# Kernel tuning notes

Measured on AMD Instinct MI355X. Metric: run time of the kernel, lower is better.

## Reference

```python
import jax, jax.numpy as jnp
import numpy as np

FORGET_BIAS = 1.0

def _lstm_step(c, h, x, W, b):
    # TF BasicLSTMCell: concat([x, h]) @ W + b -> split into i, j, f, o
    gates = jnp.concatenate([x, h], axis=-1) @ W + b
    i, j, f, o = jnp.split(gates, 4, axis=-1)
    new_c = c * jax.nn.sigmoid(f + FORGET_BIAS) + jax.nn.sigmoid(i) * jnp.tanh(j)
    new_h = jnp.tanh(new_c) * jax.nn.sigmoid(o)
    return new_c, new_h

def setup_inputs() -> dict:
    key = jax.random.key(0)
    ks = jax.random.split(key, 8)
    B, T, D, H, C = 64, 128, 2048, 512, 101
    s1 = 1.0 / np.sqrt(D + H)
    s2 = 1.0 / np.sqrt(2 * H)
    so = 1.0 / np.sqrt(H)
    return {
        "inputs": jax.random.normal(ks[0], (B, T, D), dtype=jnp.float32),
        "labels": jax.random.randint(ks[1], (B, T), 0, C, dtype=jnp.int64),
        "W1": jax.random.normal(ks[2], (D + H, 4 * H), dtype=jnp.float32) * s1,
        "b1": jnp.zeros((4 * H,), dtype=jnp.float32),
        "W2": jax.random.normal(ks[3], (2 * H, 4 * H), dtype=jnp.float32) * s2,
        "b2": jnp.zeros((4 * H,), dtype=jnp.float32),
        "Wout": jax.random.normal(ks[4], (H, C), dtype=jnp.float32) * so,
        "bout": jnp.zeros((C,), dtype=jnp.float32),
    }

def reference(inputs, labels, W1, b1, W2, b2, Wout, bout):
    B, T, D = inputs.shape
    H = Wout.shape[0]

    def step(carry, x_t):
        (c1, h1), (c2, h2) = carry
        c1, h1 = _lstm_step(c1, h1, x_t, W1, b1)
        c2, h2 = _lstm_step(c2, h2, h1, W2, b2)
        return ((c1, h1), (c2, h2)), h2

    zeros = jnp.zeros((B, H), dtype=inputs.dtype)
    init = ((zeros, zeros), (zeros, zeros))
    xs = jnp.swapaxes(inputs, 0, 1)  # [T, B, D]
    _, hs = jax.lax.scan(step, init, xs)  # hs: [T, B, H]
    outputs = jnp.swapaxes(hs, 0, 1)  # [B, T, H]

    logits = outputs @ Wout + bout  # [B, T, C]
    preds = jax.nn.softmax(logits, axis=-1)
    log_probs = jax.nn.log_softmax(logits, axis=-1)
    ce = -jnp.take_along_axis(log_probs, labels[..., None], axis=-1)[..., 0]  # [B, T]
    cost = jnp.mean(jnp.sum(ce, axis=1))
    return preds, cost
```

## Files before the change

### kernel.cpp

```cpp
#include <hip/hip_runtime.h>
#include <cmath>

#define Bb   64
#define Tt   128
#define Dd   2048
#define Hh   512
#define Gg   2048
#define Cc   101
#define PC   112
#define ROWS 8192

typedef unsigned short u16;
typedef __attribute__((ext_vector_type(8))) short bf16x8;
typedef __attribute__((ext_vector_type(4))) float f32x4;

__device__ __forceinline__ u16 bf16rne(float x) {
  unsigned u = __float_as_uint(x);
  unsigned r = (u + 0x7fffu + ((u >> 16) & 1u)) >> 16;
  return (u16)r;
}
__device__ __forceinline__ void split_bf16(float x, u16& h, u16& l) {
  h = bf16rne(x);
  l = bf16rne(x - __uint_as_float(((unsigned)h) << 16));
}
__device__ __forceinline__ float sigm(float x) { return 1.f / (1.f + expf(-x)); }

__global__ __launch_bounds__(256)
void convert_hilo(const float* __restrict__ src, u16* __restrict__ hi,
                  u16* __restrict__ lo, int n4) {
  for (int i = blockIdx.x * 256 + threadIdx.x; i < n4; i += gridDim.x * 256) {
    const float4 v = ((const float4*)src)[i];
    ushort4 h, l;
    split_bf16(v.x, h.x, l.x);
    split_bf16(v.y, h.y, l.y);
    split_bf16(v.z, h.z, l.z);
    split_bf16(v.w, h.w, l.w);
    ((ushort4*)hi)[i] = h;
    ((ushort4*)lo)[i] = l;
  }
}

__global__ __launch_bounds__(256)
void convertT_w1(const float* __restrict__ W1, u16* __restrict__ Th,
                 u16* __restrict__ Tl) {
  __shared__ float tl[32][33];
  const int tx = threadIdx.x, ty = threadIdx.y;
  const int k0 = blockIdx.x * 32, c0 = blockIdx.y * 32;
#pragma unroll
  for (int j = 0; j < 4; ++j)
    tl[ty + j * 8][tx] = W1[(size_t)(k0 + ty + j * 8) * Gg + (c0 + tx)];
  __syncthreads();
#pragma unroll
  for (int j = 0; j < 4; ++j) {
    const float v = tl[tx][ty + j * 8];
    u16 h, l;
    split_bf16(v, h, l);
    const size_t o = (size_t)(c0 + ty + j * 8) * Dd + (k0 + tx);
    Th[o] = h;
    Tl[o] = l;
  }
}

__global__ __launch_bounds__(256)
void convert_woutT(const float* __restrict__ Wout, u16* __restrict__ Th,
                   u16* __restrict__ Tl) {
  const int c = blockIdx.x;
  for (int k = threadIdx.x; k < Hh; k += 256) {
    const float v = (c < Cc) ? Wout[k * Cc + c] : 0.f;
    u16 h, l;
    split_bf16(v, h, l);
    Th[c * Hh + k] = h;
    Tl[c * Hh + k] = l;
  }
}

__global__ __launch_bounds__(256)
void permuteW(const float* __restrict__ src, u16* __restrict__ dh,
              u16* __restrict__ dl, int K) {
  __shared__ float tl[32][33];
  const int tx = threadIdx.x, ty = threadIdx.y;
  const int k0 = blockIdx.x * 32, c0 = blockIdx.y * 32;
#pragma unroll
  for (int j = 0; j < 4; ++j)
    tl[ty + j * 8][tx] = src[(size_t)(k0 + ty + j * 8) * Gg + (c0 + tx)];
  __syncthreads();
#pragma unroll
  for (int j = 0; j < 4; ++j) {
    const int col = c0 + ty + j * 8;
    const int g = col >> 9, mg = col & 511;
    const int cg = mg >> 2, m = mg & 3;
    const float v = tl[tx][ty + j * 8];
    u16 h, l;
    split_bf16(v, h, l);
    const size_t o = (size_t)(cg * 16 + g * 4 + m) * K + k0 + tx;
    dh[o] = h;
    dl[o] = l;
  }
}

__global__ __launch_bounds__(256)
void gemm1_mfma(const u16* __restrict__ Ah, const u16* __restrict__ Al,
                const u16* __restrict__ Bh, const u16* __restrict__ Bl,
                const float* __restrict__ bias, float* __restrict__ C) {
  __shared__ u16 Ash[128][40];
  __shared__ u16 Asl[128][40];
  __shared__ u16 Bsh[128][40];
  __shared__ u16 Bsl[128][40];
  const int tid  = threadIdx.x;
  const int lane = tid & 63, wave = tid >> 6;
  const int wm = wave >> 1, wn = wave & 1;
  const int l15 = lane & 15, k8 = (lane >> 4) * 8, r4 = (lane >> 4) * 4;
  const int row0 = blockIdx.y * 128, col0 = blockIdx.x * 128;
  const int srow = tid >> 1, sk = (tid & 1) * 16;

  const u16* pAh = Ah + (size_t)(row0 + srow) * Dd + sk;
  const u16* pAl = Al + (size_t)(row0 + srow) * Dd + sk;
  const u16* pBh = Bh + (size_t)(col0 + srow) * Dd + sk;
  const u16* pBl = Bl + (size_t)(col0 + srow) * Dd + sk;

  f32x4 acc[4][4];
#pragma unroll
  for (int i = 0; i < 4; ++i)
#pragma unroll
    for (int j = 0; j < 4; ++j) acc[i][j] = (f32x4){0.f, 0.f, 0.f, 0.f};

  for (int k0 = 0; k0 < Dd; k0 += 32) {
    *(bf16x8*)(&Ash[srow][sk])     = *(const bf16x8*)(pAh + k0);
    *(bf16x8*)(&Ash[srow][sk + 8]) = *(const bf16x8*)(pAh + k0 + 8);
    *(bf16x8*)(&Asl[srow][sk])     = *(const bf16x8*)(pAl + k0);
    *(bf16x8*)(&Asl[srow][sk + 8]) = *(const bf16x8*)(pAl + k0 + 8);
    *(bf16x8*)(&Bsh[srow][sk])     = *(const bf16x8*)(pBh + k0);
    *(bf16x8*)(&Bsh[srow][sk + 8]) = *(const bf16x8*)(pBh + k0 + 8);
    *(bf16x8*)(&Bsl[srow][sk])     = *(const bf16x8*)(pBl + k0);
    *(bf16x8*)(&Bsl[srow][sk + 8]) = *(const bf16x8*)(pBl + k0 + 8);
    __syncthreads();

    bf16x8 afh[4], afl[4], bfh[4], bfl[4];
#pragma unroll
    for (int mt = 0; mt < 4; ++mt) {
      afh[mt] = *(const bf16x8*)(&Ash[wm * 64 + mt * 16 + l15][k8]);
      afl[mt] = *(const bf16x8*)(&Asl[wm * 64 + mt * 16 + l15][k8]);
    }
#pragma unroll
    for (int nt = 0; nt < 4; ++nt) {
      bfh[nt] = *(const bf16x8*)(&Bsh[wn * 64 + nt * 16 + l15][k8]);
      bfl[nt] = *(const bf16x8*)(&Bsl[wn * 64 + nt * 16 + l15][k8]);
    }
#pragma unroll
    for (int mt = 0; mt < 4; ++mt)
#pragma unroll
      for (int nt = 0; nt < 4; ++nt) {
        acc[mt][nt] = __builtin_amdgcn_mfma_f32_16x16x32_bf16(
            afh[mt], bfh[nt], acc[mt][nt], 0, 0, 0);
        acc[mt][nt] = __builtin_amdgcn_mfma_f32_16x16x32_bf16(
            afh[mt], bfl[nt], acc[mt][nt], 0, 0, 0);
        acc[mt][nt] = __builtin_amdgcn_mfma_f32_16x16x32_bf16(
            afl[mt], bfh[nt], acc[mt][nt], 0, 0, 0);
      }
    __syncthreads();
  }

#pragma unroll
  for (int nt = 0; nt < 4; ++nt) {
    const int col = col0 + wn * 64 + nt * 16 + l15;
    const float bj = bias[col];
#pragma unroll
    for (int mt = 0; mt < 4; ++mt) {
      float* Cp = C + (size_t)(row0 + wm * 64 + mt * 16 + r4) * Gg + col;
#pragma unroll
      for (int r = 0; r < 4; ++r)
        Cp[(size_t)r * Gg] = acc[mt][nt][r] + bj;
    }
  }
}

__global__ __launch_bounds__(256)
void gemm_proj(const u16* __restrict__ Ah, const u16* __restrict__ Al,
               const u16* __restrict__ Bh, const u16* __restrict__ Bl,
               const float* __restrict__ bout, float* __restrict__ logits) {
  __shared__ u16 Ash[128][40];
  __shared__ u16 Asl[128][40];
  __shared__ u16 Bsh[PC][40];
  __shared__ u16 Bsl[PC][40];
  const int tid  = threadIdx.x;
  const int lane = tid & 63, wave = tid >> 6;
  const int l15 = lane & 15, k8 = (lane >> 4) * 8, r4 = (lane >> 4) * 4;
  const int row0 = blockIdx.x * 128;
  const int srow = tid >> 1, sk = (tid & 1) * 16;

  const u16* pAh = Ah + (size_t)(row0 + srow) * Hh + sk;
  const u16* pAl = Al + (size_t)(row0 + srow) * Hh + sk;
  const u16* pBh = Bh + (size_t)srow * Hh + sk;
  const u16* pBl = Bl + (size_t)srow * Hh + sk;

  f32x4 acc[2][7];
#pragma unroll
  for (int i = 0; i < 2; ++i)
#pragma unroll
    for (int j = 0; j < 7; ++j) acc[i][j] = (f32x4){0.f, 0.f, 0.f, 0.f};

  for (int k0 = 0; k0 < Hh; k0 += 32) {
    *(bf16x8*)(&Ash[srow][sk])     = *(const bf16x8*)(pAh + k0);
    *(bf16x8*)(&Ash[srow][sk + 8]) = *(const bf16x8*)(pAh + k0 + 8);
    *(bf16x8*)(&Asl[srow][sk])     = *(const bf16x8*)(pAl + k0);
    *(bf16x8*)(&Asl[srow][sk + 8]) = *(const bf16x8*)(pAl + k0 + 8);
    if (srow < PC) {
      *(bf16x8*)(&Bsh[srow][sk])     = *(const bf16x8*)(pBh + k0);
      *(bf16x8*)(&Bsh[srow][sk + 8]) = *(const bf16x8*)(pBh + k0 + 8);
      *(bf16x8*)(&Bsl[srow][sk])     = *(const bf16x8*)(pBl + k0);
      *(bf16x8*)(&Bsl[srow][sk + 8]) = *(const bf16x8*)(pBl + k0 + 8);
    }
    __syncthreads();

    bf16x8 afh[2], afl[2], bfh[7], bfl[7];
#pragma unroll
    for (int mt = 0; mt < 2; ++mt) {
      afh[mt] = *(const bf16x8*)(&Ash[wave * 32 + mt * 16 + l15][k8]);
      afl[mt] = *(const bf16x8*)(&Asl[wave * 32 + mt * 16 + l15][k8]);
    }
#pragma unroll
    for (int nt = 0; nt < 7; ++nt) {
      bfh[nt] = *(const bf16x8*)(&Bsh[nt * 16 + l15][k8]);
      bfl[nt] = *(const bf16x8*)(&Bsl[nt * 16 + l15][k8]);
    }
#pragma unroll
    for (int mt = 0; mt < 2; ++mt)
#pragma unroll
      for (int nt = 0; nt < 7; ++nt) {
        acc[mt][nt] = __builtin_amdgcn_mfma_f32_16x16x32_bf16(
            afh[mt], bfh[nt], acc[mt][nt], 0, 0, 0);
        acc[mt][nt] = __builtin_amdgcn_mfma_f32_16x16x32_bf16(
            afh[mt], bfl[nt], acc[mt][nt], 0, 0, 0);
        acc[mt][nt] = __builtin_amdgcn_mfma_f32_16x16x32_bf16(
            afl[mt], bfh[nt], acc[mt][nt], 0, 0, 0);
      }
    __syncthreads();
  }

#pragma unroll
  for (int nt = 0; nt < 7; ++nt) {
    const int col = nt * 16 + l15;
    const float bj = (col < Cc) ? bout[col] : 0.f;
#pragma unroll
    for (int mt = 0; mt < 2; ++mt) {
      float* Lp = logits + (size_t)(row0 + wave * 32 + mt * 16 + r4) * PC + col;
#pragma unroll
      for (int r = 0; r < 4; ++r)
        Lp[(size_t)r * PC] = acc[mt][nt][r] + bj;
    }
  }
}

__global__ __launch_bounds__(256)
void softmax_ce(const float* __restrict__ logits, const int* __restrict__ labels,
                float* __restrict__ preds, float* __restrict__ ce) {
  const int lane = threadIdx.x & 63, wv = threadIdx.x >> 6;
  const int row = blockIdx.x * 4 + wv;
  const float* lg = logits + (size_t)row * PC;
  const bool a0 = (lane < Cc), a1 = (lane + 64 < Cc);
  const float v0 = a0 ? lg[lane] : -INFINITY;
  const float v1 = a1 ? lg[lane + 64] : -INFINITY;
  float m = fmaxf(v0, v1);
#pragma unroll
  for (int off = 32; off > 0; off >>= 1) m = fmaxf(m, __shfl_xor(m, off));
  const float e0 = a0 ? expf(v0 - m) : 0.f;
  const float e1 = a1 ? expf(v1 - m) : 0.f;
  float s = e0 + e1;
#pragma unroll
  for (int off = 32; off > 0; off >>= 1) s += __shfl_xor(s, off);
  if (a0) preds[(size_t)row * Cc + lane] = e0 / s;
  if (a1) preds[(size_t)row * Cc + lane + 64] = e1 / s;
  const int lab = labels[row];
  if (lab == lane)           ce[row] = logf(s) + m - v0;
  else if (lab == lane + 64) ce[row] = logf(s) + m - v1;
}

#define BM 128
#define BN 128
#define BK 16

__global__ __launch_bounds__(256)
void sgemm_bias(const float* __restrict__ A, const float* __restrict__ B,
                const float* __restrict__ bias, float* __restrict__ C,
                int M, int N, int K) {
  __shared__ float As[BK][BM];
  __shared__ float Bs[BK][BN];
  const int tid  = threadIdx.x;
  const int row0 = blockIdx.y * BM, col0 = blockIdx.x * BN;
  const int tr = (tid >> 4) << 3;
  const int tc = (tid & 15) << 3;

  float acc[8][8];
#pragma unroll
  for (int i = 0; i < 8; ++i)
#pragma unroll
    for (int j = 0; j < 8; ++j) acc[i][j] = 0.f;

  const int arow = tid >> 1;
  const int acol = (tid & 1) << 3;
  const int brow = tid >> 4;
  const int bcol = (tid & 15) << 3;
  const float* Ap = A + (size_t)(row0 + arow) * K + acol;
  const float* Bp = B + (size_t)brow * N + (col0 + bcol);

  for (int k0 = 0; k0 < K; k0 += BK) {
    const float4 a0 = *(const float4*)(Ap + k0);
    const float4 a1 = *(const float4*)(Ap + k0 + 4);
    const float4 bv0 = *(const float4*)(Bp + (size_t)k0 * N);
    const float4 bv1 = *(const float4*)(Bp + (size_t)k0 * N + 4);
    As[acol + 0][arow] = a0.x;
    As[acol + 1][arow] = a0.y;
    As[acol + 2][arow] = a0.z;
    As[acol + 3][arow] = a0.w;
    As[acol + 4][arow] = a1.x;
    As[acol + 5][arow] = a1.y;
    As[acol + 6][arow] = a1.z;
    As[acol + 7][arow] = a1.w;
    *(float4*)(&Bs[brow][bcol])     = bv0;
    *(float4*)(&Bs[brow][bcol + 4]) = bv1;
    __syncthreads();
#pragma unroll
    for (int k = 0; k < BK; ++k) {
      float a[8], b[8];
      *(float4*)(a)     = *(const float4*)(&As[k][tr]);
      *(float4*)(a + 4) = *(const float4*)(&As[k][tr + 4]);
      *(float4*)(b)     = *(const float4*)(&Bs[k][tc]);
      *(float4*)(b + 4) = *(const float4*)(&Bs[k][tc + 4]);
#pragma unroll
      for (int i = 0; i < 8; ++i)
#pragma unroll
        for (int j = 0; j < 8; ++j)
          acc[i][j] = fmaf(a[i], b[j], acc[i][j]);
    }
    __syncthreads();
  }

  float bj[8];
#pragma unroll
  for (int j = 0; j < 8; ++j) bj[j] = bias[col0 + tc + j];
#pragma unroll
  for (int i = 0; i < 8; ++i) {
    float* Cp = C + (size_t)(row0 + tr + i) * N + (col0 + tc);
    float4 o0, o1;
    o0.x = acc[i][0] + bj[0]; o0.y = acc[i][1] + bj[1];
    o0.z = acc[i][2] + bj[2]; o0.w = acc[i][3] + bj[3];
    o1.x = acc[i][4] + bj[4]; o1.y = acc[i][5] + bj[5];
    o1.z = acc[i][6] + bj[6]; o1.w = acc[i][7] + bj[7];
    *(float4*)(Cp)     = o0;
    *(float4*)(Cp + 4) = o1;
  }
}

__global__ __launch_bounds__(256, 2)
void fused_step3(const float* __restrict__ pre,
                 const u16* __restrict__ WP1h, const u16* __restrict__ WP1l,
                 const u16* __restrict__ WP2h, const u16* __restrict__ WP2l,
                 const float* __restrict__ b2,
                 u16* __restrict__ h1hi, u16* __restrict__ h1lo,
                 u16* __restrict__ h2hi, u16* __restrict__ h2lo,
                 u16* __restrict__ h2fh, u16* __restrict__ h2fl,
                 float* __restrict__ c1, float* __restrict__ c2, int t) {
  __shared__ u16 Ah[2][32][136], Al[2][32][136];
  __shared__ u16 Bh[2][16][136], Bl[2][16][136];
  __shared__ float ex[2][2][16][17];
  const int tid = threadIdx.x;
  const int lane = tid & 63, w = tid >> 6;
  const int bt = w & 1, kh = w >> 1;
  const int fr = lane & 15, f8 = (lane >> 4) * 8, r4 = (lane >> 4) * 4;
  const bool isL2 = blockIdx.x >= 256;
  const int idx = blockIdx.x & 255;
  const int cg = idx & 127, bg = idx >> 7;
  const int b0 = bg * 32;

  const int hr = tid >> 3, hk = (tid & 7) * 16;
  const int wv = tid >> 4, wk = (tid & 15) * 8;

  f32x4 acc = {0.f, 0.f, 0.f, 0.f};
  bool have = false;
  float p0 = 0.f, p1 = 0.f, p2 = 0.f, p3 = 0.f;

  const int eb = tid >> 2, em = tid & 3;
  const int col = cg * 4 + em;
  const int ci = (b0 + eb) * Hh + col;

  if (!isL2) {
    if (t >= Tt) return;
    if (tid < 128) {
      const float* pp = pre + ((size_t)(b0 + eb) * Tt + t) * Gg + col;
      p0 = pp[0]; p1 = pp[512]; p2 = pp[1024]; p3 = pp[1536];
    }
    if (t > 0) {
      const int sl = (t - 1) & 1;
      const u16* A_h = h1hi + (sl << 15) + (b0 + hr) * 512 + hk;
      const u16* A_l = h1lo + (sl << 15) + (b0 + hr) * 512 + hk;
      const u16* B_h = WP1h + (size_t)(cg * 16 + wv) * 512 + wk;
      const u16* B_l = WP1l + (size_t)(cg * 16 + wv) * 512 + wk;

      bf16x8 ra0, ra1, rl0, rl1, rwh, rwl;
      ra0 = *(const bf16x8*)(A_h);     ra1 = *(const bf16x8*)(A_h + 8);
      rl0 = *(const bf16x8*)(A_l);     rl1 = *(const bf16x8*)(A_l + 8);
      rwh = *(const bf16x8*)(B_h);     rwl = *(const bf16x8*)(B_l);
      *(bf16x8*)&Ah[0][hr][hk] = ra0;  *(bf16x8*)&Ah[0][hr][hk + 8] = ra1;
      *(bf16x8*)&Al[0][hr][hk] = rl0;  *(bf16x8*)&Al[0][hr][hk + 8] = rl1;
      *(bf16x8*)&Bh[0][wv][wk] = rwh;  *(bf16x8*)&Bl[0][wv][wk] = rwl;
      __syncthreads();

      for (int kc = 0; kc < 4; ++kc) {
        const int cur = kc & 1;
        if (kc < 3) {
          const int ko = (kc + 1) * 128;
          ra0 = *(const bf16x8*)(A_h + ko);     ra1 = *(const bf16x8*)(A_h + ko + 8);
          rl0 = *(const bf16x8*)(A_l + ko);     rl1 = *(const bf16x8*)(A_l + ko + 8);
          rwh = *(const bf16x8*)(B_h + ko);     rwl = *(const bf16x8*)(B_l + ko);
        }
#pragma unroll
        for (int s = 0; s < 2; ++s) {
          const int c0 = kh * 64 + s * 32 + f8;
          const bf16x8 afh = *(const bf16x8*)&Ah[cur][bt * 16 + fr][c0];
          const bf16x8 afl = *(const bf16x8*)&Al[cur][bt * 16 + fr][c0];
          const bf16x8 bfh = *(const bf16x8*)&Bh[cur][fr][c0];
          const bf16x8 bfl = *(const bf16x8*)&Bl[cur][fr][c0];
          acc = __builtin_amdgcn_mfma_f32_16x16x32_bf16(afh, bfh, acc, 0, 0, 0);
          acc = __builtin_amdgcn_mfma_f32_16x16x32_bf16(afh, bfl, acc, 0, 0, 0);
          acc = __builtin_amdgcn_mfma_f32_16x16x32_bf16(afl, bfh, acc, 0, 0, 0);
        }
        if (kc < 3) {
          const int nb = cur ^ 1;
          *(bf16x8*)&Ah[nb][hr][hk] = ra0;  *(bf16x8*)&Ah[nb][hr][hk + 8] = ra1;
          *(bf16x8*)&Al[nb][hr][hk] = rl0;  *(bf16x8*)&Al[nb][hr][hk + 8] = rl1;
          *(bf16x8*)&Bh[nb][wv][wk] = rwh;  *(bf16x8*)&Bl[nb][wv][wk] = rwl;
        }
        __syncthreads();
      }
      have = true;
    }
  } else {
    if (t < 1) return;
    const u16* A1h = h1hi + (((t - 1) & 1) << 15) + (b0 + hr) * 512 + hk;
    const u16* A1l = h1lo + (((t - 1) & 1) << 15) + (b0 + hr) * 512 + hk;
    const u16* A2h = h2hi + (((t - 2) & 1) << 15) + (b0 + hr) * 512 + hk;
    const u16* A2l = h2lo + (((t - 2) & 1) << 15) + (b0 + hr) * 512 + hk;
    const u16* B_h = WP2h + (size_t)(cg * 16 + wv) * 1024 + wk;
    const u16* B_l = WP2l + (size_t)(cg * 16 + wv) * 1024 + wk;
    const bool h2ok = (t >= 2);

    bf16x8 ra0, ra1, rl0, rl1, rwh, rwl;
    ra0 = *(const bf16x8*)(A1h);     ra1 = *(const bf16x8*)(A1h + 8);
    rl0 = *(const bf16x8*)(A1l);     rl1 = *(const bf16x8*)(A1l + 8);
    rwh = *(const bf16x8*)(B_h);     rwl = *(const bf16x8*)(B_l);
    *(bf16x8*)&Ah[0][hr][hk] = ra0;  *(bf16x8*)&Ah[0][hr][hk + 8] = ra1;
    *(bf16x8*)&Al[0][hr][hk] = rl0;  *(bf16x8*)&Al[0][hr][hk + 8] = rl1;
    *(bf16x8*)&Bh[0][wv][wk] = rwh;  *(bf16x8*)&Bl[0][wv][wk] = rwl;
    __syncthreads();

    for (int kc = 0; kc < 8; ++kc) {
      const int cur = kc & 1;
      if (kc < 7) {
        const int nk = kc + 1;
        const u16* sh  = (nk < 4) ? A1h : A2h;
        const u16* sl2 = (nk < 4) ? A1l : A2l;
        const int ko = (nk & 3) * 128;
        ra0 = *(const bf16x8*)(sh + ko);      ra1 = *(const bf16x8*)(sh + ko + 8);
        rl0 = *(const bf16x8*)(sl2 + ko);     rl1 = *(const bf16x8*)(sl2 + ko + 8);
        rwh = *(const bf16x8*)(B_h + nk * 128);
        rwl = *(const bf16x8*)(B_l + nk * 128);
      }
      if (kc < 4 || h2ok) {
#pragma unroll
        for (int s = 0; s < 2; ++s) {
          const int c0 = kh * 64 + s * 32 + f8;
          const bf16x8 afh = *(const bf16x8*)&Ah[cur][bt * 16 + fr][c0];
          const bf16x8 afl = *(const bf16x8*)&Al[cur][bt * 16 + fr][c0];
          const bf16x8 bfh = *(const bf16x8*)&Bh[cur][fr][c0];
          const bf16x8 bfl = *(const bf16x8*)&Bl[cur][fr][c0];
          acc = __builtin_amdgcn_mfma_f32_16x16x32_bf16(afh, bfh, acc, 0, 0, 0);
          acc = __builtin_amdgcn_mfma_f32_16x16x32_bf16(afh, bfl, acc, 0, 0, 0);
          acc = __builtin_amdgcn_mfma_f32_16x16x32_bf16(afl, bfh, acc, 0, 0, 0);
        }
      }
      if (kc < 7) {
        const int nb = cur ^ 1;
        *(bf16x8*)&Ah[nb][hr][hk] = ra0;  *(bf16x8*)&Ah[nb][hr][hk + 8] = ra1;
        *(bf16x8*)&Al[nb][hr][hk] = rl0;  *(bf16x8*)&Al[nb][hr][hk + 8] = rl1;
        *(bf16x8*)&Bh[nb][wv][wk] = rwh;  *(bf16x8*)&Bl[nb][wv][wk] = rwl;
      }
      __syncthreads();
    }
    have = true;
  }

  if (have) {
#pragma unroll
    for (int r = 0; r < 4; ++r)
      ex[kh][bt][r4 + r][fr] = acc[r];
  }
  __syncthreads();

  if (tid < 128) {
    const int bte = eb >> 4, bl = eb & 15;
    float s0 = 0.f, s1 = 0.f, s2 = 0.f, s3 = 0.f;
    if (have) {
      s0 = ex[0][bte][bl][0 + em] + ex[1][bte][bl][0 + em];
      s1 = ex[0][bte][bl][4 + em] + ex[1][bte][bl][4 + em];
      s2 = ex[0][bte][bl][8 + em] + ex[1][bte][bl][8 + em];
      s3 = ex[0][bte][bl][12 + em] + ex[1][bte][bl][12 + em];
    }
    if (!isL2) {
      const float gi = p0 + s0, gj = p1 + s1, gf = p2 + s2, go = p3 + s3;
      const float cp = (t > 0) ? c1[ci] : 0.f;
      const float nc = fmaf(cp, sigm(gf + 1.f), sigm(gi) * tanhf(gj));
      c1[ci] = nc;
      const float nh = tanhf(nc) * sigm(go);
      u16 hh, hl;
      split_bf16(nh, hh, hl);
      const int hidx = ((t & 1) << 15) + ci;
      h1hi[hidx] = hh;
      h1lo[hidx] = hl;
    } else {
      const float gi = b2[col] + s0, gj = b2[512 + col] + s1;
      const float gf = b2[1024 + col] + s2, go = b2[1536 + col] + s3;
      const float cp = (t >= 2) ? c2[ci] : 0.f;
      const float nc = fmaf(cp, sigm(gf + 1.f), sigm(gi) * tanhf(gj));
      c2[ci] = nc;
      const float nh = tanhf(nc) * sigm(go);
      u16 hh, hl;
      split_bf16(nh, hh, hl);
      const int hidx = (((t - 1) & 1) << 15) + ci;
      h2hi[hidx] = hh;
      h2lo[hidx] = hl;
      const size_t fo = ((size_t)(b0 + eb) * Tt + (t - 1)) * Hh + col;
      h2fh[fo] = hh;
      h2fl[fo] = hl;
    }
  }
}

__global__ __launch_bounds__(256)
void reduce_cost(const float* __restrict__ ce, float* __restrict__ out) {
  __shared__ float red[256];
  const int tid = threadIdx.x;
  float s = 0.f;
  for (int i = tid; i < ROWS; i += 256) s += ce[i];
  red[tid] = s;
  __syncthreads();
  for (int st = 128; st > 0; st >>= 1) {
    if (tid < st) red[tid] += red[tid + st];
    __syncthreads();
  }
  if (tid == 0) out[0] = red[0] / (float)Bb;
}

extern "C" void kernel_launch(void* const* d_in, const int* in_sizes, int n_in,
                              void* d_out, int out_size, void* d_ws, size_t ws_size,
                              hipStream_t stream) {
  const float* inputs = (const float*)d_in[0];
  const int*   labels = (const int*)d_in[1];
  const float* W1     = (const float*)d_in[2];
  const float* b1     = (const float*)d_in[3];
  const float* W2     = (const float*)d_in[4];
  const float* b2     = (const float*)d_in[5];
  const float* Wout   = (const float*)d_in[6];
  const float* bout   = (const float*)d_in[7];
  float* out = (float*)d_out;

  float* ws     = (float*)d_ws;
  float* pre    = ws;
  float* c1     = pre    + (size_t)ROWS * Gg;
  float* c2     = c1     + (size_t)Bb * Hh;
  float* ceb    = c2     + (size_t)Bb * Hh;
  float* logits = ceb    + ROWS;
  u16* h1hi = (u16*)(logits + (size_t)ROWS * PC);
  u16* h1lo = h1hi + 2 * 64 * 512;
  u16* h2hi = h1lo + 2 * 64 * 512;
  u16* h2lo = h2hi + 2 * 64 * 512;
  u16* h2fh = h2lo + 2 * 64 * 512;
  u16* h2fl = h2fh + (size_t)ROWS * Hh;
  u16* WP1h = h2fl + (size_t)ROWS * Hh;
  u16* WP1l = WP1h + 128 * 16 * 512;
  u16* WP2h = WP1l + 128 * 16 * 512;
  u16* WP2l = WP2h + 128 * 16 * 1024;
  u16* WoTh = WP2l + 128 * 16 * 1024;
  u16* WoTl = WoTh + PC * Hh;
  u16* Xhi  = WoTl + PC * Hh;
  u16* Xlo  = Xhi  + (size_t)ROWS * Dd;
  u16* W1Th = Xlo  + (size_t)ROWS * Dd;
  u16* W1Tl = W1Th + (size_t)Gg * Dd;
  const size_t need = (size_t)((char*)(W1Tl + (size_t)Gg * Dd) - (char*)d_ws);
  const bool use_mfma = ws_size >= need;

  permuteW<<<dim3(16, 64), dim3(32, 8), 0, stream>>>(
      W1 + (size_t)Dd * Gg, WP1h, WP1l, 512);
  permuteW<<<dim3(32, 64), dim3(32, 8), 0, stream>>>(W2, WP2h, WP2l, 1024);
  convert_woutT<<<PC, 256, 0, stream>>>(Wout, WoTh, WoTl);

  if (use_mfma) {
    convert_hilo<<<2048, 256, 0, stream>>>(inputs, Xhi, Xlo, ROWS * Dd / 4);
    convertT_w1<<<dim3(64, 64), dim3(32, 8), 0, stream>>>(W1, W1Th, W1Tl);
    gemm1_mfma<<<dim3(Gg / 128, ROWS / 128), 256, 0, stream>>>(
        Xhi, Xlo, W1Th, W1Tl, b1, pre);
  } else {
    sgemm_bias<<<dim3(Gg / BN, ROWS / BM), dim3(256), 0, stream>>>(
        inputs, W1, b1, pre, ROWS, Gg, Dd);
  }

  for (int t = 0; t <= Tt; ++t)
    fused_step3<<<512, 256, 0, stream>>>(pre, WP1h, WP1l, WP2h, WP2l, b2,
                                         h1hi, h1lo, h2hi, h2lo,
                                         h2fh, h2fl, c1, c2, t);

  gemm_proj<<<ROWS / 128, 256, 0, stream>>>(h2fh, h2fl, WoTh, WoTl, bout, logits);
  softmax_ce<<<ROWS / 4, 256, 0, stream>>>(logits, labels, out, ceb);
  reduce_cost<<<1, 256, 0, stream>>>(ceb, out + (size_t)ROWS * Cc);
}
```

Before: 1.529 ms.

## Split recurrent step blocks to 16 batch rows with 4-way K split

```diff
diff --git a/kernel.cpp b/kernel.cpp
--- a/kernel.cpp
+++ b/kernel.cpp
@@ -351,8 +351,8 @@
   }
 }
 
-__global__ __launch_bounds__(256, 2)
-void fused_step3(const float* __restrict__ pre,
+__global__ __launch_bounds__(256, 4)
+void fused_step4(const float* __restrict__ pre,
                  const u16* __restrict__ WP1h, const u16* __restrict__ WP1l,
                  const u16* __restrict__ WP2h, const u16* __restrict__ WP2l,
                  const float* __restrict__ b2,
@@ -360,20 +360,18 @@
                  u16* __restrict__ h2hi, u16* __restrict__ h2lo,
                  u16* __restrict__ h2fh, u16* __restrict__ h2fl,
                  float* __restrict__ c1, float* __restrict__ c2, int t) {
-  __shared__ u16 Ah[2][32][136], Al[2][32][136];
+  __shared__ u16 Ah[2][16][136], Al[2][16][136];
   __shared__ u16 Bh[2][16][136], Bl[2][16][136];
-  __shared__ float ex[2][2][16][17];
+  __shared__ float ex[4][16][17];
   const int tid = threadIdx.x;
-  const int lane = tid & 63, w = tid >> 6;
-  const int bt = w & 1, kh = w >> 1;
+  const int lane = tid & 63, kh = tid >> 6;
   const int fr = lane & 15, f8 = (lane >> 4) * 8, r4 = (lane >> 4) * 4;
-  const bool isL2 = blockIdx.x >= 256;
-  const int idx = blockIdx.x & 255;
+  const bool isL2 = blockIdx.x >= 512;
+  const int idx = blockIdx.x & 511;
   const int cg = idx & 127, bg = idx >> 7;
-  const int b0 = bg * 32;
-
-  const int hr = tid >> 3, hk = (tid & 7) * 16;
-  const int wv = tid >> 4, wk = (tid & 15) * 8;
+  const int b0 = bg * 16;
+
+  const int hr = tid >> 4, hk = (tid & 15) * 8;
 
   f32x4 acc = {0.f, 0.f, 0.f, 0.f};
   bool have = false;
@@ -385,7 +383,7 @@
 
   if (!isL2) {
     if (t >= Tt) return;
-    if (tid < 128) {
+    if (tid < 64) {
       const float* pp = pre + ((size_t)(b0 + eb) * Tt + t) * Gg + col;
       p0 = pp[0]; p1 = pp[512]; p2 = pp[1024]; p3 = pp[1536];
     }
@@ -393,31 +391,27 @@
       const int sl = (t - 1) & 1;
       const u16* A_h = h1hi + (sl << 15) + (b0 + hr) * 512 + hk;
       const u16* A_l = h1lo + (sl << 15) + (b0 + hr) * 512 + hk;
-      const u16* B_h = WP1h + (size_t)(cg * 16 + wv) * 512 + wk;
-      const u16* B_l = WP1l + (size_t)(cg * 16 + wv) * 512 + wk;
-
-      bf16x8 ra0, ra1, rl0, rl1, rwh, rwl;
-      ra0 = *(const bf16x8*)(A_h);     ra1 = *(const bf16x8*)(A_h + 8);
-      rl0 = *(const bf16x8*)(A_l);     rl1 = *(const bf16x8*)(A_l + 8);
-      rwh = *(const bf16x8*)(B_h);     rwl = *(const bf16x8*)(B_l);
-      *(bf16x8*)&Ah[0][hr][hk] = ra0;  *(bf16x8*)&Ah[0][hr][hk + 8] = ra1;
-      *(bf16x8*)&Al[0][hr][hk] = rl0;  *(bf16x8*)&Al[0][hr][hk + 8] = rl1;
-      *(bf16x8*)&Bh[0][wv][wk] = rwh;  *(bf16x8*)&Bl[0][wv][wk] = rwl;
+      const u16* B_h = WP1h + (size_t)(cg * 16 + hr) * 512 + hk;
+      const u16* B_l = WP1l + (size_t)(cg * 16 + hr) * 512 + hk;
+
+      bf16x8 ra, rl_, rbh, rbl;
+      ra = *(const bf16x8*)(A_h);   rl_ = *(const bf16x8*)(A_l);
+      rbh = *(const bf16x8*)(B_h);  rbl = *(const bf16x8*)(B_l);
+      *(bf16x8*)&Ah[0][hr][hk] = ra;   *(bf16x8*)&Al[0][hr][hk] = rl_;
+      *(bf16x8*)&Bh[0][hr][hk] = rbh;  *(bf16x8*)&Bl[0][hr][hk] = rbl;
       __syncthreads();
 
       for (int kc = 0; kc < 4; ++kc) {
         const int cur = kc & 1;
         if (kc < 3) {
           const int ko = (kc + 1) * 128;
-          ra0 = *(const bf16x8*)(A_h + ko);     ra1 = *(const bf16x8*)(A_h + ko + 8);
-          rl0 = *(const bf16x8*)(A_l + ko);     rl1 = *(const bf16x8*)(A_l + ko + 8);
-          rwh = *(const bf16x8*)(B_h + ko);     rwl = *(const bf16x8*)(B_l + ko);
+          ra = *(const bf16x8*)(A_h + ko);   rl_ = *(const bf16x8*)(A_l + ko);
+          rbh = *(const bf16x8*)(B_h + ko);  rbl = *(const bf16x8*)(B_l + ko);
         }
-#pragma unroll
-        for (int s = 0; s < 2; ++s) {
-          const int c0 = kh * 64 + s * 32 + f8;
-          const bf16x8 afh = *(const bf16x8*)&Ah[cur][bt * 16 + fr][c0];
-          const bf16x8 afl = *(const bf16x8*)&Al[cur][bt * 16 + fr][c0];
+        {
+          const int c0 = kh * 32 + f8;
+          const bf16x8 afh = *(const bf16x8*)&Ah[cur][fr][c0];
+          const bf16x8 afl = *(const bf16x8*)&Al[cur][fr][c0];
           const bf16x8 bfh = *(const bf16x8*)&Bh[cur][fr][c0];
           const bf16x8 bfl = *(const bf16x8*)&Bl[cur][fr][c0];
           acc = __builtin_amdgcn_mfma_f32_16x16x32_bf16(afh, bfh, acc, 0, 0, 0);
@@ -426,9 +420,8 @@
         }
         if (kc < 3) {
           const int nb = cur ^ 1;
-          *(bf16x8*)&Ah[nb][hr][hk] = ra0;  *(bf16x8*)&Ah[nb][hr][hk + 8] = ra1;
-          *(bf16x8*)&Al[nb][hr][hk] = rl0;  *(bf16x8*)&Al[nb][hr][hk + 8] = rl1;
-          *(bf16x8*)&Bh[nb][wv][wk] = rwh;  *(bf16x8*)&Bl[nb][wv][wk] = rwl;
+          *(bf16x8*)&Ah[nb][hr][hk] = ra;   *(bf16x8*)&Al[nb][hr][hk] = rl_;
+          *(bf16x8*)&Bh[nb][hr][hk] = rbh;  *(bf16x8*)&Bl[nb][hr][hk] = rbl;
         }
         __syncthreads();
       }
@@ -440,17 +433,15 @@
     const u16* A1l = h1lo + (((t - 1) & 1) << 15) + (b0 + hr) * 512 + hk;
     const u16* A2h = h2hi + (((t - 2) & 1) << 15) + (b0 + hr) * 512 + hk;
     const u16* A2l = h2lo + (((t - 2) & 1) << 15) + (b0 + hr) * 512 + hk;
-    const u16* B_h = WP2h + (size_t)(cg * 16 + wv) * 1024 + wk;
-    const u16* B_l = WP2l + (size_t)(cg * 16 + wv) * 1024 + wk;
+    const u16* B_h = WP2h + (size_t)(cg * 16 + hr) * 1024 + hk;
+    const u16* B_l = WP2l + (size_t)(cg * 16 + hr) * 1024 + hk;
     const bool h2ok = (t >= 2);
 
-    bf16x8 ra0, ra1, rl0, rl1, rwh, rwl;
-    ra0 = *(const bf16x8*)(A1h);     ra1 = *(const bf16x8*)(A1h + 8);
-    rl0 = *(const bf16x8*)(A1l);     rl1 = *(const bf16x8*)(A1l + 8);
-    rwh = *(const bf16x8*)(B_h);     rwl = *(const bf16x8*)(B_l);
-    *(bf16x8*)&Ah[0][hr][hk] = ra0;  *(bf16x8*)&Ah[0][hr][hk + 8] = ra1;
-    *(bf16x8*)&Al[0][hr][hk] = rl0;  *(bf16x8*)&Al[0][hr][hk + 8] = rl1;
-    *(bf16x8*)&Bh[0][wv][wk] = rwh;  *(bf16x8*)&Bl[0][wv][wk] = rwl;
+    bf16x8 ra, rl_, rbh, rbl;
+    ra = *(const bf16x8*)(A1h);   rl_ = *(const bf16x8*)(A1l);
+    rbh = *(const bf16x8*)(B_h);  rbl = *(const bf16x8*)(B_l);
+    *(bf16x8*)&Ah[0][hr][hk] = ra;   *(bf16x8*)&Al[0][hr][hk] = rl_;
+    *(bf16x8*)&Bh[0][hr][hk] = rbh;  *(bf16x8*)&Bl[0][hr][hk] = rbl;
     __syncthreads();
 
     for (int kc = 0; kc < 8; ++kc) {
@@ -460,29 +451,24 @@
         const u16* sh  = (nk < 4) ? A1h : A2h;
         const u16* sl2 = (nk < 4) ? A1l : A2l;
         const int ko = (nk & 3) * 128;
-        ra0 = *(const bf16x8*)(sh + ko);      ra1 = *(const bf16x8*)(sh + ko + 8);
-        rl0 = *(const bf16x8*)(sl2 + ko);     rl1 = *(const bf16x8*)(sl2 + ko + 8);
-        rwh = *(const bf16x8*)(B_h + nk * 128);
-        rwl = *(const bf16x8*)(B_l + nk * 128);
+        ra = *(const bf16x8*)(sh + ko);    rl_ = *(const bf16x8*)(sl2 + ko);
+        rbh = *(const bf16x8*)(B_h + nk * 128);
+        rbl = *(const bf16x8*)(B_l + nk * 128);
       }
       if (kc < 4 || h2ok) {
-#pragma unroll
-        for (int s = 0; s < 2; ++s) {
-          const int c0 = kh * 64 + s * 32 + f8;
-          const bf16x8 afh = *(const bf16x8*)&Ah[cur][bt * 16 + fr][c0];
-          const bf16x8 afl = *(const bf16x8*)&Al[cur][bt * 16 + fr][c0];
-          const bf16x8 bfh = *(const bf16x8*)&Bh[cur][fr][c0];
-          const bf16x8 bfl = *(const bf16x8*)&Bl[cur][fr][c0];
-          acc = __builtin_amdgcn_mfma_f32_16x16x32_bf16(afh, bfh, acc, 0, 0, 0);
-          acc = __builtin_amdgcn_mfma_f32_16x16x32_bf16(afh, bfl, acc, 0, 0, 0);
-          acc = __builtin_amdgcn_mfma_f32_16x16x32_bf16(afl, bfh, acc, 0, 0, 0);
-        }
+        const int c0 = kh * 32 + f8;
+        const bf16x8 afh = *(const bf16x8*)&Ah[cur][fr][c0];
+        const bf16x8 afl = *(const bf16x8*)&Al[cur][fr][c0];
+        const bf16x8 bfh = *(const bf16x8*)&Bh[cur][fr][c0];
+        const bf16x8 bfl = *(const bf16x8*)&Bl[cur][fr][c0];
+        acc = __builtin_amdgcn_mfma_f32_16x16x32_bf16(afh, bfh, acc, 0, 0, 0);
+        acc = __builtin_amdgcn_mfma_f32_16x16x32_bf16(afh, bfl, acc, 0, 0, 0);
+        acc = __builtin_amdgcn_mfma_f32_16x16x32_bf16(afl, bfh, acc, 0, 0, 0);
       }
       if (kc < 7) {
         const int nb = cur ^ 1;
-        *(bf16x8*)&Ah[nb][hr][hk] = ra0;  *(bf16x8*)&Ah[nb][hr][hk + 8] = ra1;
-        *(bf16x8*)&Al[nb][hr][hk] = rl0;  *(bf16x8*)&Al[nb][hr][hk + 8] = rl1;
-        *(bf16x8*)&Bh[nb][wv][wk] = rwh;  *(bf16x8*)&Bl[nb][wv][wk] = rwl;
+        *(bf16x8*)&Ah[nb][hr][hk] = ra;   *(bf16x8*)&Al[nb][hr][hk] = rl_;
+        *(bf16x8*)&Bh[nb][hr][hk] = rbh;  *(bf16x8*)&Bl[nb][hr][hk] = rbl;
       }
       __syncthreads();
     }
@@ -492,18 +478,20 @@
   if (have) {
 #pragma unroll
     for (int r = 0; r < 4; ++r)
-      ex[kh][bt][r4 + r][fr] = acc[r];
+      ex[kh][r4 + r][fr] = acc[r];
   }
   __syncthreads();
 
-  if (tid < 128) {
-    const int bte = eb >> 4, bl = eb & 15;
+  if (tid < 64) {
     float s0 = 0.f, s1 = 0.f, s2 = 0.f, s3 = 0.f;
     if (have) {
-      s0 = ex[0][bte][bl][0 + em] + ex[1][bte][bl][0 + em];
-      s1 = ex[0][bte][bl][4 + em] + ex[1][bte][bl][4 + em];
-      s2 = ex[0][bte][bl][8 + em] + ex[1][bte][bl][8 + em];
-      s3 = ex[0][bte][bl][12 + em] + ex[1][bte][bl][12 + em];
+#pragma unroll
+      for (int q = 0; q < 4; ++q) {
+        s0 += ex[q][eb][0 + em];
+        s1 += ex[q][eb][4 + em];
+        s2 += ex[q][eb][8 + em];
+        s3 += ex[q][eb][12 + em];
+      }
     }
     if (!isL2) {
       const float gi = p0 + s0, gj = p1 + s1, gf = p2 + s2, go = p3 + s3;
@@ -604,9 +592,9 @@
   }
 
   for (int t = 0; t <= Tt; ++t)
-    fused_step3<<<512, 256, 0, stream>>>(pre, WP1h, WP1l, WP2h, WP2l, b2,
-                                         h1hi, h1lo, h2hi, h2lo,
-                                         h2fh, h2fl, c1, c2, t);
+    fused_step4<<<1024, 256, 0, stream>>>(pre, WP1h, WP1l, WP2h, WP2l, b2,
+                                          h1hi, h1lo, h2hi, h2lo,
+                                          h2fh, h2fl, c1, c2, t);
 
   gemm_proj<<<ROWS / 128, 256, 0, stream>>>(h2fh, h2fl, WoTh, WoTl, bout, logits);
   softmax_ce<<<ROWS / 4, 256, 0, stream>>>(logits, labels, out, ceb);
```

Result: no change. 1.520 ms (-0.5%).
